# Optimization experiments

Measured on AMD Instinct MI355X. Metric: run time of the kernel, lower is better.

## Reference

```python
import jax, jax.numpy as jnp
import numpy as np

N, NW, M, H, C = 16384, 512, 32, 8, 16
T_SEG, N_SIG = 512, 3


def _forward(query_feats, key_feats, value_feats, query_table, key_table,
             value_table, table_offsets, win_indices, table_idx):
    # gather voxels into windows: [nW, M, H, C]
    q = query_feats[win_indices]
    k = key_feats[win_indices]
    v = value_feats[win_indices]
    # base attention coefficients: [nW, H, M, M]
    logits = jnp.einsum('wihc,wjhc->whij', q, k)
    n_sig = table_idx.shape[-1]
    for s in range(n_sig):  # fixed, small signal loop (xyz cRSE)
        idx_s = table_offsets[s] + table_idx[..., s]      # [nW, M, M]
        tq = query_table[idx_s]                            # [nW, M, M, H, C]
        tk = key_table[idx_s]
        logits = logits + jnp.einsum('wihc,wijhc->whij', q, tq) \
                        + jnp.einsum('wjhc,wijhc->whij', k, tk)
    # max-stabilized exp (cal_max_coffs + self_attn_forward)
    rmax = jnp.max(logits, axis=-1, keepdims=True)
    ecoff = jnp.exp(logits - rmax)                         # [nW, H, M, M]
    sum_coffs = jnp.sum(ecoff, axis=-1)                    # [nW, H, M]
    raw = jnp.einsum('whij,wjhc->wihc', ecoff, v)          # [nW, M, H, C]
    for s in range(n_sig):
        idx_s = table_offsets[s] + table_idx[..., s]
        tv = value_table[idx_s]
        raw = raw + jnp.einsum('whij,wijhc->wihc', ecoff, tv)
    norm = raw / jnp.transpose(sum_coffs, (0, 2, 1))[..., None]
    # scatter windows back to voxel order (win_indices is a permutation)
    out = jnp.zeros_like(query_feats).at[win_indices.reshape(-1)].set(
        norm.reshape(-1, norm.shape[-2], norm.shape[-1]))
    return out


def setup_inputs() -> dict:
    key = jax.random.key(0)
    ks = jax.random.split(key, 9)
    feats = lambda k: jax.random.normal(k, (N, H, C), dtype=jnp.float32)
    table = lambda k: 0.02 * jax.random.normal(k, (N_SIG * T_SEG, H, C), dtype=jnp.float32)
    win_indices = jax.random.permutation(ks[6], N).reshape(NW, M).astype(jnp.int32)
    table_idx = jax.random.randint(ks[7], (NW, M, M, N_SIG), 0, T_SEG, dtype=jnp.int32)
    table_offsets = (jnp.arange(N_SIG, dtype=jnp.int32) * T_SEG)
    return {
        'query_feats': feats(ks[0]), 'key_feats': feats(ks[1]), 'value_feats': feats(ks[2]),
        'query_table': table(ks[3]), 'key_table': table(ks[4]), 'value_table': table(ks[5]),
        'table_offsets': table_offsets, 'win_indices': win_indices, 'table_idx': table_idx,
    }


def reference(query_feats, key_feats, value_feats, query_table, key_table,
              value_table, table_offsets, win_indices, table_idx):
    return _forward(query_feats, key_feats, value_feats, query_table, key_table,
                    value_table, table_offsets, win_indices, table_idx)
```

## Files before the change

### kernel.cpp

```cpp
#include <hip/hip_runtime.h>

namespace {
constexpr int NWIN = 512;
constexpr int M    = 32;
constexpr int H    = 8;
constexpr int C    = 16;
constexpr int NSIG = 3;
constexpr int HC   = H * C;
constexpr int HB   = 4;
constexpr int HBC  = HB * C;
}

__device__ __forceinline__ float dot4(const float4& a, const float4& b) {
  return a.x * b.x + a.y * b.y + a.z * b.z + a.w * b.w;
}
__device__ __forceinline__ const float4* f4p(const float* p) {
  return reinterpret_cast<const float4*>(p);
}

__global__ __launch_bounds__(256, 4)
void win_attn(const float* __restrict__ qf, const float* __restrict__ kf,
              const float* __restrict__ vf, const float* __restrict__ qt,
              const float* __restrict__ kt, const float* __restrict__ vt,
              const int* __restrict__ toff, const int* __restrict__ widx,
              const int* __restrict__ tidx, float* __restrict__ out)
{
  const int w  = blockIdx.x >> 1;
  const int hb = (blockIdx.x & 1) * HB;
  const int t  = threadIdx.x;
  const int hl = t >> 6;
  const int ch = (t >> 5) & 1;
  const int i  = t & 31;
  const int h  = hb + hl;
  const int cb = ch * 8;

  __shared__ float k_lds[M][HBC];
  __shared__ float v_lds[M][HBC];
  __shared__ int   tid_lds[M * NSIG * M];
  __shared__ int   vox_lds[M];
  __shared__ int   off_lds[NSIG];

  if (t < M)    vox_lds[t] = widx[w * M + t];
  if (t < NSIG) off_lds[t] = toff[t];
  __syncthreads();

  #pragma unroll
  for (int r = 0; r < 2; ++r) {
    const int flat = t + 256 * r;
    const int j    = flat >> 4;
    const int f4i  = (flat & 15) * 4;
    const int goff = vox_lds[j] * HC + hb * C + f4i;
    *reinterpret_cast<float4*>(&k_lds[j][f4i]) = *f4p(kf + goff);
    *reinterpret_cast<float4*>(&v_lds[j][f4i]) = *f4p(vf + goff);
  }
  #pragma unroll
  for (int r = 0; r < 12; ++r) {
    const int g   = t + 256 * r;
    const int ii  = g / 96;
    const int rem = g - ii * 96;
    const int jj  = rem / 3;
    const int ss  = rem - jj * 3;
    tid_lds[(jj * NSIG + ss) * M + ii] = tidx[w * (M * M * NSIG) + g];
  }

  const int vox_i = vox_lds[i];
  const float* qrow = qf + vox_i * HC + h * C + cb;
  const float4 q0 = f4p(qrow)[0], q1 = f4p(qrow)[1];
  const int offs[NSIG] = { off_lds[0], off_lds[1], off_lds[2] };
  __syncthreads();

  float lg[M];
  #pragma unroll
  for (int j = 0; j < M; ++j) {
    const float* krow = &k_lds[j][hl * C + cb];
    const float4 k0 = f4p(krow)[0], k1 = f4p(krow)[1];
    float acc = dot4(q0, k0) + dot4(q1, k1);
    #pragma unroll
    for (int s = 0; s < NSIG; ++s) {
      const int row = offs[s] + tid_lds[(j * NSIG + s) * M + i];
      const float* tqr = qt + row * HC + h * C + cb;
      acc += dot4(q0, f4p(tqr)[0]) + dot4(q1, f4p(tqr)[1]);
      const float* tkr = kt + row * HC + h * C + cb;
      acc += dot4(k0, f4p(tkr)[0]) + dot4(k1, f4p(tkr)[1]);
    }
    acc += __shfl_xor(acc, 32);
    lg[j] = acc;
  }

  float m = lg[0];
  #pragma unroll
  for (int j = 1; j < M; ++j) m = fmaxf(m, lg[j]);
  float ssum = 0.f;
  #pragma unroll
  for (int j = 0; j < M; ++j) { lg[j] = expf(lg[j] - m); ssum += lg[j]; }

  float oacc[8];
  #pragma unroll
  for (int c = 0; c < 8; ++c) oacc[c] = 0.f;
  #pragma unroll
  for (int j = 0; j < M; ++j) {
    const float e = lg[j];
    const float* vrow = &v_lds[j][hl * C + cb];
    #pragma unroll
    for (int c4 = 0; c4 < 2; ++c4) {
      const float4 vv = f4p(vrow)[c4];
      oacc[4 * c4 + 0] += e * vv.x;
      oacc[4 * c4 + 1] += e * vv.y;
      oacc[4 * c4 + 2] += e * vv.z;
      oacc[4 * c4 + 3] += e * vv.w;
    }
    #pragma unroll
    for (int s = 0; s < NSIG; ++s) {
      const int row = offs[s] + tid_lds[(j * NSIG + s) * M + i];
      const float* tvr = vt + row * HC + h * C + cb;
      #pragma unroll
      for (int c4 = 0; c4 < 2; ++c4) {
        const float4 tv = f4p(tvr)[c4];
        oacc[4 * c4 + 0] += e * tv.x;
        oacc[4 * c4 + 1] += e * tv.y;
        oacc[4 * c4 + 2] += e * tv.z;
        oacc[4 * c4 + 3] += e * tv.w;
      }
    }
  }

  const float inv = 1.0f / ssum;
  float* orow = out + vox_i * HC + h * C + cb;
  #pragma unroll
  for (int c4 = 0; c4 < 2; ++c4) {
    float4 o;
    o.x = oacc[4 * c4 + 0] * inv;
    o.y = oacc[4 * c4 + 1] * inv;
    o.z = oacc[4 * c4 + 2] * inv;
    o.w = oacc[4 * c4 + 3] * inv;
    *reinterpret_cast<float4*>(orow + 4 * c4) = o;
  }
}

extern "C" void kernel_launch(void* const* d_in, const int* in_sizes, int n_in,
                              void* d_out, int out_size, void* d_ws, size_t ws_size,
                              hipStream_t stream) {
  (void)in_sizes; (void)n_in; (void)d_ws; (void)ws_size; (void)out_size;
  const float* qf  = (const float*)d_in[0];
  const float* kf  = (const float*)d_in[1];
  const float* vf  = (const float*)d_in[2];
  const float* qt  = (const float*)d_in[3];
  const float* kt  = (const float*)d_in[4];
  const float* vt  = (const float*)d_in[5];
  const int*  toff = (const int*)d_in[6];
  const int*  widx = (const int*)d_in[7];
  const int*  tidx = (const int*)d_in[8];
  float* out = (float*)d_out;
  win_attn<<<NWIN * 2, 256, 0, stream>>>(qf, kf, vf, qt, kt, vt, toff, widx, tidx, out);
}
```

Before: 413.6 us.

## Fuse logit and value passes with online softmax and combined value-table sum

```diff
diff --git a/kernel.cpp b/kernel.cpp
--- a/kernel.cpp
+++ b/kernel.cpp
@@ -69,72 +69,66 @@
   const int offs[NSIG] = { off_lds[0], off_lds[1], off_lds[2] };
   __syncthreads();
 
-  float lg[M];
+  float m    = -INFINITY;
+  float ssum = 0.f;
+  float oacc[8];
+  #pragma unroll
+  for (int c = 0; c < 8; ++c) oacc[c] = 0.f;
+
   #pragma unroll
   for (int j = 0; j < M; ++j) {
     const float* krow = &k_lds[j][hl * C + cb];
     const float4 k0 = f4p(krow)[0], k1 = f4p(krow)[1];
-    float acc = dot4(q0, k0) + dot4(q1, k1);
+    const float4 vv0 = f4p(&v_lds[j][hl * C + cb])[0];
+    const float4 vv1 = f4p(&v_lds[j][hl * C + cb])[1];
+
+    float logit = dot4(q0, k0) + dot4(q1, k1);
+    float4 tv0[NSIG], tv1[NSIG];
     #pragma unroll
     for (int s = 0; s < NSIG; ++s) {
       const int row = offs[s] + tid_lds[(j * NSIG + s) * M + i];
-      const float* tqr = qt + row * HC + h * C + cb;
-      acc += dot4(q0, f4p(tqr)[0]) + dot4(q1, f4p(tqr)[1]);
-      const float* tkr = kt + row * HC + h * C + cb;
-      acc += dot4(k0, f4p(tkr)[0]) + dot4(k1, f4p(tkr)[1]);
+      const float* base = qt + row * HC + h * C + cb;
+      const float4 a0 = f4p(base)[0], a1 = f4p(base)[1];
+      const float* kbase = kt + row * HC + h * C + cb;
+      const float4 b0 = f4p(kbase)[0], b1 = f4p(kbase)[1];
+      const float* vbase = vt + row * HC + h * C + cb;
+      tv0[s] = f4p(vbase)[0];
+      tv1[s] = f4p(vbase)[1];
+      logit += dot4(q0, a0) + dot4(q1, a1) + dot4(k0, b0) + dot4(k1, b1);
     }
-    acc += __shfl_xor(acc, 32);
-    lg[j] = acc;
-  }
+    logit += __shfl_xor(logit, 32);
 
-  float m = lg[0];
-  #pragma unroll
-  for (int j = 1; j < M; ++j) m = fmaxf(m, lg[j]);
-  float ssum = 0.f;
-  #pragma unroll
-  for (int j = 0; j < M; ++j) { lg[j] = expf(lg[j] - m); ssum += lg[j]; }
+    const float mnew  = fmaxf(m, logit);
+    const float scale = expf(m - mnew);
+    const float e     = expf(logit - mnew);
+    ssum = ssum * scale + e;
+    m    = mnew;
 
-  float oacc[8];
-  #pragma unroll
-  for (int c = 0; c < 8; ++c) oacc[c] = 0.f;
-  #pragma unroll
-  for (int j = 0; j < M; ++j) {
-    const float e = lg[j];
-    const float* vrow = &v_lds[j][hl * C + cb];
-    #pragma unroll
-    for (int c4 = 0; c4 < 2; ++c4) {
-      const float4 vv = f4p(vrow)[c4];
-      oacc[4 * c4 + 0] += e * vv.x;
-      oacc[4 * c4 + 1] += e * vv.y;
-      oacc[4 * c4 + 2] += e * vv.z;
-      oacc[4 * c4 + 3] += e * vv.w;
-    }
-    #pragma unroll
-    for (int s = 0; s < NSIG; ++s) {
-      const int row = offs[s] + tid_lds[(j * NSIG + s) * M + i];
-      const float* tvr = vt + row * HC + h * C + cb;
-      #pragma unroll
-      for (int c4 = 0; c4 < 2; ++c4) {
-        const float4 tv = f4p(tvr)[c4];
-        oacc[4 * c4 + 0] += e * tv.x;
-        oacc[4 * c4 + 1] += e * tv.y;
-        oacc[4 * c4 + 2] += e * tv.z;
-        oacc[4 * c4 + 3] += e * tv.w;
-      }
-    }
+    float4 sv0 = tv0[0], sv1 = tv1[0];
+    sv0.x += tv0[1].x + tv0[2].x + vv0.x;  sv0.y += tv0[1].y + tv0[2].y + vv0.y;
+    sv0.z += tv0[1].z + tv0[2].z + vv0.z;  sv0.w += tv0[1].w + tv0[2].w + vv0.w;
+    sv1.x += tv1[1].x + tv1[2].x + vv1.x;  sv1.y += tv1[1].y + tv1[2].y + vv1.y;
+    sv1.z += tv1[1].z + tv1[2].z + vv1.z;  sv1.w += tv1[1].w + tv1[2].w + vv1.w;
+
+    oacc[0] = oacc[0] * scale + e * sv0.x;
+    oacc[1] = oacc[1] * scale + e * sv0.y;
+    oacc[2] = oacc[2] * scale + e * sv0.z;
+    oacc[3] = oacc[3] * scale + e * sv0.w;
+    oacc[4] = oacc[4] * scale + e * sv1.x;
+    oacc[5] = oacc[5] * scale + e * sv1.y;
+    oacc[6] = oacc[6] * scale + e * sv1.z;
+    oacc[7] = oacc[7] * scale + e * sv1.w;
   }
 
   const float inv = 1.0f / ssum;
   float* orow = out + vox_i * HC + h * C + cb;
-  #pragma unroll
-  for (int c4 = 0; c4 < 2; ++c4) {
-    float4 o;
-    o.x = oacc[4 * c4 + 0] * inv;
-    o.y = oacc[4 * c4 + 1] * inv;
-    o.z = oacc[4 * c4 + 2] * inv;
-    o.w = oacc[4 * c4 + 3] * inv;
-    *reinterpret_cast<float4*>(orow + 4 * c4) = o;
-  }
+  float4 o0, o1;
+  o0.x = oacc[0] * inv;  o0.y = oacc[1] * inv;
+  o0.z = oacc[2] * inv;  o0.w = oacc[3] * inv;
+  o1.x = oacc[4] * inv;  o1.y = oacc[5] * inv;
+  o1.z = oacc[6] * inv;  o1.w = oacc[7] * inv;
+  reinterpret_cast<float4*>(orow)[0] = o0;
+  reinterpret_cast<float4*>(orow)[1] = o1;
 }
 
 extern "C" void kernel_launch(void* const* d_in, const int* in_sizes, int n_in,
```

Result: faster. 351.7 us (-15.0%).
